# Kernel optimization log

Measured on AMD Instinct MI355X. Metric: run time of the kernel, lower is better.

Reference implementation:

```python
import jax, jax.numpy as jnp
import numpy as np

ATT = 512  # attention_size

def setup_inputs() -> dict:
    key = jax.random.key(0)
    k0, k1, k2, k3, k4 = jax.random.split(key, 5)
    B, Sq, Sk, Din, Dmem = 32, 1024, 1024, 512, 512
    inputs = jax.random.normal(k0, (B, Sq, Din), dtype=jnp.float32)
    memory = jax.random.normal(k1, (B, Sk, Dmem), dtype=jnp.float32)
    memory_mask = jax.random.randint(k2, (B, Sk), 0, 2).astype(jnp.int32)
    W_input = (jax.random.normal(k3, (Din, ATT), dtype=jnp.float32) * 0.02)
    W_memory = (jax.random.normal(k4, (Dmem, ATT), dtype=jnp.float32) * 0.02)
    return {"inputs": inputs, "memory": memory, "memory_mask": memory_mask,
            "W_input": W_input, "W_memory": W_memory}

def reference(inputs, memory, memory_mask, W_input, W_memory):
    # projections (bias=False) + ReLU; dropout=0 -> identity
    x = jax.nn.relu(jnp.einsum('bqd,da->bqa', inputs, W_input))   # [B,Sq,A]
    m = jax.nn.relu(jnp.einsum('bkd,da->bka', memory, W_memory))  # [B,Sk,A]
    scale = 1.0 / jnp.sqrt(jnp.asarray(ATT, dtype=inputs.dtype))
    logits = jnp.einsum('bqa,bka->bqk', x, m) * scale             # [B,Sq,Sk]
    mask = (memory_mask[:, None, :] != 0)                         # [B,1,Sk] broadcast over Sq
    logits = jnp.where(mask, logits, jnp.asarray(-1e30, dtype=logits.dtype))
    score = jax.nn.softmax(logits, axis=-1)
    context = jnp.einsum('bqk,bkd->bqd', score, memory)           # [B,Sq,Dmem]
    return jnp.concatenate([context, inputs], axis=-1)            # [B,Sq,Dmem+Din]
```

## Files before the change

### kernel.cpp

```cpp
#include <hip/hip_runtime.h>

typedef __bf16 bf16x8 __attribute__((ext_vector_type(8)));
typedef float f32x4 __attribute__((ext_vector_type(4)));

__device__ __forceinline__ unsigned short f2bf(float f) {
    union { float f; unsigned u; } v; v.f = f;
    unsigned r = v.u + 0x7FFFu + ((v.u >> 16) & 1u);
    return (unsigned short)(r >> 16);
}

__global__ __launch_bounds__(256) void prep_kernel(
    const float4* __restrict__ inputs4, uint2* __restrict__ InB16,
    float4* __restrict__ out4,
    const float* __restrict__ W0, const float* __restrict__ W1,
    unsigned short* __restrict__ D0, unsigned short* __restrict__ D1,
    const int* __restrict__ mask, int* __restrict__ kidx,
    int* __restrict__ cnt, int* __restrict__ padded,
    float4* __restrict__ rowsum4)
{
    __shared__ float tile[32][33];
    __shared__ int wsum[4];
    const int bid = blockIdx.x;
    const int t = threadIdx.x;

    if (bid < 16384) {
        const int i = bid * 256 + t;
        const int bq = i >> 7;
        const int d  = i & 127;
        float4 v = inputs4[i];
        out4[(size_t)bq * 256 + 128 + d] = v;
        union { unsigned short u[4]; uint2 p; } pk;
        pk.u[0] = f2bf(v.x); pk.u[1] = f2bf(v.y);
        pk.u[2] = f2bf(v.z); pk.u[3] = f2bf(v.w);
        InB16[i] = pk.p;
    } else if (bid < 16896) {
        const int tb = bid - 16384;
        const float* src = (tb >> 8) ? W1 : W0;
        unsigned short* dst = (tb >> 8) ? D1 : D0;
        const int rem = tb & 255;
        const int s0 = (rem & 15) * 32, d0 = (rem >> 4) * 32;
        const int tr = t >> 5, tc = t & 31;
#pragma unroll
        for (int i = 0; i < 4; i++)
            tile[tr + i * 8][tc] = src[(size_t)(s0 + tr + i * 8) * 512 + d0 + tc];
        __syncthreads();
#pragma unroll
        for (int i = 0; i < 4; i++)
            dst[(size_t)(d0 + tr + i * 8) * 512 + s0 + tc] = f2bf(tile[tc][tr + i * 8]);
    } else {
        const int b = bid - 16896;
        rowsum4[b * 256 + t] = float4{0.f, 0.f, 0.f, 0.f};
        const int* m = mask + b * 1024;
        int v[4]; int s = 0;
#pragma unroll
        for (int e = 0; e < 4; e++) { v[e] = (m[t * 4 + e] != 0) ? 1 : 0; s += v[e]; }
        const int lane = t & 63, wv = t >> 6;
        int x = s;
#pragma unroll
        for (int off = 1; off < 64; off <<= 1) {
            int y = __shfl_up(x, off, 64);
            if (lane >= off) x += y;
        }
        if (lane == 63) wsum[wv] = x;
        __syncthreads();
        int base = 0;
        for (int w = 0; w < wv; w++) base += wsum[w];
        int pos = base + x - s;
#pragma unroll
        for (int e = 0; e < 4; e++)
            if (v[e]) kidx[b * 1024 + pos++] = t * 4 + e;
        if (t == 255) {
            int total = base + x;
            cnt[b] = total;
            padded[b] = (total + 127) & ~127;
        }
    }
}

__global__ __launch_bounds__(256) void gather_mem_kernel(
    const float* __restrict__ memory, const int* __restrict__ kidx,
    const int* __restrict__ cnt, const int* __restrict__ padded,
    unsigned short* __restrict__ MemG, unsigned short* __restrict__ MemGT)
{
    const int b = blockIdx.z;
    const int j0 = blockIdx.x * 32, d0 = blockIdx.y * 32;
    if (j0 >= padded[b]) return;
    const int nb = cnt[b];
    __shared__ float tile[32][33];
    const float* src = memory + (size_t)b * 1024 * 512;
    const int t = threadIdx.x, tr = t >> 5, tc = t & 31;
#pragma unroll
    for (int i = 0; i < 4; i++) {
        int j = j0 + tr + i * 8;
        float v = 0.f;
        if (j < nb) v = src[(size_t)kidx[b * 1024 + j] * 512 + d0 + tc];
        tile[tr + i * 8][tc] = v;
        MemG[(size_t)b * 1024 * 512 + (size_t)j * 512 + d0 + tc] = f2bf(v);
    }
    __syncthreads();
#pragma unroll
    for (int i = 0; i < 4; i++) {
        int d = d0 + tr + i * 8;
        MemGT[(size_t)b * 512 * 1024 + (size_t)d * 1024 + j0 + tc] = f2bf(tile[tc][tr + i * 8]);
    }
}

template<int CMODE>
__device__ __forceinline__ void gemm_core(
    unsigned char* lds,
    const unsigned short* __restrict__ Ab, const unsigned short* __restrict__ Bb,
    void* __restrict__ Cb, float* __restrict__ rs, int nbv,
    int rowA, int rowB, int Kz, int lda, int ldb, int ldc, float scale)
{
    const int nt = Kz >> 6;

    const int t = threadIdx.x;
    const int w = t >> 6;
    const int lane = t & 63;
    const int wm = w >> 2;
    const int wn = w & 3;
    const int l15 = lane & 15;
    const int sx = (((lane >> 4) ^ ((l15 >> 1) & 3)) << 4);

    const int r0 = t >> 2;
    const int sl = (t & 3) ^ ((t >> 3) & 3);
    const unsigned short* aS0 = Ab + (size_t)(rowA + r0) * lda + sl * 8;
    const unsigned short* aS1 = aS0 + (size_t)128 * lda;
    const unsigned short* bS0 = Bb + (size_t)(rowB + r0) * ldb + sl * 8;
    const unsigned short* bS1 = bS0 + (size_t)128 * ldb;

    const int wofs = w * 1024;
    const int aRd = (wm * 128 + l15) * 64 + sx;
    const int bRd = 32768 + (wn * 64 + l15) * 64 + sx;

    f32x4 acc[8][4];
#pragma unroll
    for (int i = 0; i < 8; i++)
#pragma unroll
        for (int j = 0; j < 4; j++) acc[i][j] = f32x4{0.f, 0.f, 0.f, 0.f};

#define GLL(SRC, DOFS) __builtin_amdgcn_global_load_lds(                        \
        (const __attribute__((address_space(1))) void*)(SRC),                   \
        (__attribute__((address_space(3))) void*)&lds[DOFS], 16, 0, 0)
#define STAGEA(BUF, KH, KEL) do {                                               \
        GLL(aS0 + (KEL), (BUF) * 65536 + (KH) * 16384 + wofs);                  \
        GLL(aS1 + (KEL), (BUF) * 65536 + (KH) * 16384 + wofs + 8192); } while (0)
#define STAGEB(BUF, KH, KEL) do {                                               \
        GLL(bS0 + (KEL), (BUF) * 65536 + 32768 + (KH) * 16384 + wofs);          \
        GLL(bS1 + (KEL), (BUF) * 65536 + 32768 + (KH) * 16384 + wofs + 8192); } while (0)

    STAGEA(0, 0, 0); STAGEB(0, 0, 0); STAGEA(0, 1, 32); STAGEB(0, 1, 32);
    asm volatile("s_waitcnt vmcnt(4)" ::: "memory");
    __builtin_amdgcn_s_barrier();

    for (int tt = 0; tt < nt; ++tt) {
        const int cur = (tt & 1) * 65536;
        const int nxt = (tt & 1) ^ 1;
        const bool pf = (tt + 1) < nt;
        const int kn = (tt + 1) * 64;
        bf16x8 af[4], bf0[4], bf1[4];

#pragma unroll
        for (int i = 0; i < 4; i++) af[i]  = *(const bf16x8*)&lds[cur + aRd + i * 1024];
#pragma unroll
        for (int j = 0; j < 4; j++) bf0[j] = *(const bf16x8*)&lds[cur + bRd + j * 1024];
        if (pf) STAGEA(nxt, 0, kn);
        __builtin_amdgcn_s_barrier();
        asm volatile("s_waitcnt lgkmcnt(0)" ::: "memory");
        __builtin_amdgcn_sched_barrier(0);
        __builtin_amdgcn_s_setprio(1);
#pragma unroll
        for (int i = 0; i < 4; i++)
#pragma unroll
            for (int j = 0; j < 4; j++)
                acc[i][j] = __builtin_amdgcn_mfma_f32_16x16x32_bf16(af[i], bf0[j], acc[i][j], 0, 0, 0);
        __builtin_amdgcn_s_setprio(0);
        __builtin_amdgcn_s_barrier();

#pragma unroll
        for (int i = 0; i < 4; i++) af[i] = *(const bf16x8*)&lds[cur + aRd + (i + 4) * 1024];
        if (pf) STAGEB(nxt, 0, kn);
        __builtin_amdgcn_s_barrier();
        asm volatile("s_waitcnt lgkmcnt(0)" ::: "memory");
        __builtin_amdgcn_sched_barrier(0);
        __builtin_amdgcn_s_setprio(1);
#pragma unroll
        for (int i = 0; i < 4; i++)
#pragma unroll
            for (int j = 0; j < 4; j++)
                acc[i + 4][j] = __builtin_amdgcn_mfma_f32_16x16x32_bf16(af[i], bf0[j], acc[i + 4][j], 0, 0, 0);
        __builtin_amdgcn_s_setprio(0);
        if (pf) { asm volatile("s_waitcnt vmcnt(4)" ::: "memory"); }
        else    { asm volatile("s_waitcnt vmcnt(0)" ::: "memory"); }
        __builtin_amdgcn_s_barrier();

#pragma unroll
        for (int i = 0; i < 4; i++) af[i]  = *(const bf16x8*)&lds[cur + 16384 + aRd + i * 1024];
#pragma unroll
        for (int j = 0; j < 4; j++) bf1[j] = *(const bf16x8*)&lds[cur + 16384 + bRd + j * 1024];
        if (pf) STAGEA(nxt, 1, kn + 32);
        __builtin_amdgcn_s_barrier();
        asm volatile("s_waitcnt lgkmcnt(0)" ::: "memory");
        __builtin_amdgcn_sched_barrier(0);
        __builtin_amdgcn_s_setprio(1);
#pragma unroll
        for (int i = 0; i < 4; i++)
#pragma unroll
            for (int j = 0; j < 4; j++)
                acc[i][j] = __builtin_amdgcn_mfma_f32_16x16x32_bf16(af[i], bf1[j], acc[i][j], 0, 0, 0);
        __builtin_amdgcn_s_setprio(0);
        __builtin_amdgcn_s_barrier();

#pragma unroll
        for (int i = 0; i < 4; i++) af[i] = *(const bf16x8*)&lds[cur + 16384 + aRd + (i + 4) * 1024];
        if (pf) STAGEB(nxt, 1, kn + 32);
        __builtin_amdgcn_s_barrier();
        asm volatile("s_waitcnt lgkmcnt(0)" ::: "memory");
        __builtin_amdgcn_sched_barrier(0);
        __builtin_amdgcn_s_setprio(1);
#pragma unroll
        for (int i = 0; i < 4; i++)
#pragma unroll
            for (int j = 0; j < 4; j++)
                acc[i + 4][j] = __builtin_amdgcn_mfma_f32_16x16x32_bf16(af[i], bf1[j], acc[i + 4][j], 0, 0, 0);
        __builtin_amdgcn_s_setprio(0);
        if (pf) { asm volatile("s_waitcnt vmcnt(4)" ::: "memory"); }
        __builtin_amdgcn_s_barrier();
    }

#undef GLL
#undef STAGEA
#undef STAGEB

    const int orow = (lane >> 4) * 4;
    const int ocol = l15;

    if constexpr (CMODE == 0) {
        unsigned short* C = (unsigned short*)Cb;
#pragma unroll
        for (int mf = 0; mf < 8; mf++)
#pragma unroll
            for (int nf = 0; nf < 4; nf++) {
                const int col = rowB + wn * 64 + nf * 16 + ocol;
#pragma unroll
                for (int r = 0; r < 4; r++) {
                    const int rw = rowA + wm * 128 + mf * 16 + orow + r;
                    C[(size_t)rw * ldc + col] = f2bf(fmaxf(acc[mf][nf][r], 0.f));
                }
            }
    } else if constexpr (CMODE == 1) {
        unsigned short* C = (unsigned short*)Cb;
#pragma unroll
        for (int mf = 0; mf < 8; mf++) {
            float part[4] = {0.f, 0.f, 0.f, 0.f};
#pragma unroll
            for (int nf = 0; nf < 4; nf++) {
                const int col = rowB + wn * 64 + nf * 16 + ocol;
#pragma unroll
                for (int r = 0; r < 4; r++) {
                    float p = (col < nbv) ? __expf(acc[mf][nf][r] * scale) : 0.f;
                    part[r] += p;
                    const int rw = rowA + wm * 128 + mf * 16 + orow + r;
                    C[(size_t)rw * ldc + col] = f2bf(p);
                }
            }
#pragma unroll
            for (int r = 0; r < 4; r++) {
                float s = part[r];
                s += __shfl_xor(s, 1, 64);
                s += __shfl_xor(s, 2, 64);
                s += __shfl_xor(s, 4, 64);
                s += __shfl_xor(s, 8, 64);
                if (ocol == 0)
                    atomicAdd(&rs[rowA + wm * 128 + mf * 16 + orow + r], s);
            }
        }
    } else {
        float* C = (float*)Cb;
#pragma unroll
        for (int mf = 0; mf < 8; mf++) {
            float inv[4];
#pragma unroll
            for (int r = 0; r < 4; r++)
                inv[r] = 1.0f / rs[rowA + wm * 128 + mf * 16 + orow + r];
#pragma unroll
            for (int nf = 0; nf < 4; nf++) {
                const int col = rowB + wn * 64 + nf * 16 + ocol;
#pragma unroll
                for (int r = 0; r < 4; r++) {
                    const int rw = rowA + wm * 128 + mf * 16 + orow + r;
                    C[(size_t)rw * ldc + col] = acc[mf][nf][r] * inv[r];
                }
            }
        }
    }
}

__global__ __launch_bounds__(512, 2) void gemm_proj_kernel(
    const unsigned short* __restrict__ InB16, const unsigned short* __restrict__ WtIn,
    unsigned short* __restrict__ Xq,
    const unsigned short* __restrict__ MemG, const unsigned short* __restrict__ WtMem,
    unsigned short* __restrict__ Xm, const int* __restrict__ padded)
{
    __shared__ __align__(16) unsigned char lds[131072];
    const int y = blockIdx.y;
    const int rowB = blockIdx.x * 256;
    const unsigned short* A;
    const unsigned short* Bt;
    unsigned short* C;
    int rowA;
    if (y < 128) {
        A = InB16; Bt = WtIn; C = Xq; rowA = y * 256;
    } else {
        const int idx = y - 128;
        const int z = idx >> 2;
        rowA = (idx & 3) * 256;
        if (rowA >= padded[z]) return;
        A = MemG + (size_t)z * 524288;
        Bt = WtMem;
        C = Xm + (size_t)z * 524288;
    }
    gemm_core<0>(lds, A, Bt, (void*)C, nullptr, 0, rowA, rowB,
                 512, 512, 512, 512, 0.f);
}

__global__ __launch_bounds__(512, 2) void gemm_p_kernel(
    const unsigned short* __restrict__ Xq, const unsigned short* __restrict__ Xm,
    unsigned short* __restrict__ P, const int* __restrict__ cnt,
    const int* __restrict__ padded, float* __restrict__ rowsum, float scale)
{
    __shared__ __align__(16) unsigned char lds[131072];
    const int z = blockIdx.z;
    const int rowB = blockIdx.x * 256;
    if (rowB >= padded[z]) return;
    gemm_core<1>(lds, Xq + (size_t)z * 524288, Xm + (size_t)z * 524288,
                 (void*)(P + (size_t)z * 1048576), rowsum + (size_t)z * 1024, cnt[z],
                 blockIdx.y * 256, rowB, 512, 512, 512, 1024, scale);
}

__global__ __launch_bounds__(512, 2) void gemm_ctx_kernel(
    const unsigned short* __restrict__ P, const unsigned short* __restrict__ MemGT,
    float* __restrict__ out, const int* __restrict__ padded, float* __restrict__ rowsum)
{
    __shared__ __align__(16) unsigned char lds[131072];
    const int z = blockIdx.z;
    gemm_core<2>(lds, P + (size_t)z * 1048576, MemGT + (size_t)z * 524288,
                 (void*)(out + (size_t)z * 1048576), rowsum + (size_t)z * 1024, 0,
                 blockIdx.y * 256, blockIdx.x * 256, padded[z],
                 1024, 1024, 1024, 1.f);
}

extern "C" void kernel_launch(void* const* d_in, const int* in_sizes, int n_in,
                              void* d_out, int out_size, void* d_ws, size_t ws_size,
                              hipStream_t stream)
{
    const float* inputs = (const float*)d_in[0];
    const float* memory = (const float*)d_in[1];
    const int*   mmask  = (const int*)d_in[2];
    const float* W_in   = (const float*)d_in[3];
    const float* W_mem  = (const float*)d_in[4];
    float* out = (float*)d_out;

    char* ws = (char*)d_ws;
    const unsigned long long MB = 1048576ull;
    unsigned short* Wt_in  = (unsigned short*)(ws);
    unsigned short* Wt_mem = (unsigned short*)(ws + 524288);
    unsigned short* InB16  = (unsigned short*)(ws + 1 * MB);
    unsigned short* MemG   = (unsigned short*)(ws + 33 * MB);
    unsigned short* P      = (unsigned short*)(ws + 1 * MB);
    unsigned short* MemGT  = (unsigned short*)(ws + 65 * MB);
    unsigned short* Xq     = (unsigned short*)(ws + 97 * MB);
    unsigned short* Xm     = (unsigned short*)(ws + 129 * MB);
    float*          rowsum = (float*)(ws + 161 * MB);
    int*            kidx   = (int*)(ws + 161 * MB + 131072);
    int*            cntp   = (int*)(ws + 161 * MB + 262144);
    int*            padp   = (int*)(ws + 161 * MB + 262144 + 128);

    const float scale = 0.04419417382415922f;

    prep_kernel<<<16928, 256, 0, stream>>>(
        (const float4*)inputs, (uint2*)InB16, (float4*)out,
        W_in, W_mem, Wt_in, Wt_mem,
        mmask, kidx, cntp, padp, (float4*)rowsum);

    gather_mem_kernel<<<dim3(32, 16, 32), 256, 0, stream>>>(
        memory, kidx, cntp, padp, MemG, MemGT);

    gemm_proj_kernel<<<dim3(2, 256, 1), 512, 0, stream>>>(
        InB16, Wt_in, Xq, MemG, Wt_mem, Xm, padp);

    gemm_p_kernel<<<dim3(4, 4, 32), 512, 0, stream>>>(
        Xq, Xm, P, cntp, padp, rowsum, scale);

    gemm_ctx_kernel<<<dim3(2, 4, 32), 512, 0, stream>>>(
        P, MemGT, out, padp, rowsum);
}
```

Baseline: 398.6 us.

## Fuse mask compaction and memory gather into prep kernel; XCD-aware block remapping

```diff
diff --git a/kernel.cpp b/kernel.cpp
--- a/kernel.cpp
+++ b/kernel.cpp
@@ -14,17 +14,107 @@
     float4* __restrict__ out4,
     const float* __restrict__ W0, const float* __restrict__ W1,
     unsigned short* __restrict__ D0, unsigned short* __restrict__ D1,
-    const int* __restrict__ mask, int* __restrict__ kidx,
+    const int* __restrict__ mask,
     int* __restrict__ cnt, int* __restrict__ padded,
-    float4* __restrict__ rowsum4)
+    float4* __restrict__ rowsum4,
+    const float* __restrict__ memory,
+    unsigned short* __restrict__ MemG, unsigned short* __restrict__ MemGT)
 {
     __shared__ float tile[32][33];
     __shared__ int wsum[4];
+    __shared__ int kidx32[32];
     const int bid = blockIdx.x;
     const int t = threadIdx.x;
 
-    if (bid < 16384) {
-        const int i = bid * 256 + t;
+    if (bid < 1024) {
+        const int b = bid >> 5;
+        const int jt = bid & 31;
+        const int* m = mask + b * 1024;
+        int v[4]; int s = 0;
+#pragma unroll
+        for (int e = 0; e < 4; e++) { v[e] = (m[t * 4 + e] != 0) ? 1 : 0; s += v[e]; }
+        const int lane = t & 63, wv = t >> 6;
+        int x = s;
+#pragma unroll
+        for (int off = 1; off < 64; off <<= 1) {
+            int y = __shfl_up(x, off, 64);
+            if (lane >= off) x += y;
+        }
+        if (lane == 63) wsum[wv] = x;
+        __syncthreads();
+        int base = 0;
+        for (int w = 0; w < wv; w++) base += wsum[w];
+        const int nb = wsum[0] + wsum[1] + wsum[2] + wsum[3];
+        const int pb = (nb + 127) & ~127;
+        const int j0 = jt * 32;
+        if (j0 >= pb) return;
+        int pos = base + x - s;
+#pragma unroll
+        for (int e = 0; e < 4; e++)
+            if (v[e]) {
+                int p = pos++;
+                if (p >= j0 && p < j0 + 32) kidx32[p - j0] = t * 4 + e;
+            }
+        __syncthreads();
+
+        const float* src = memory + (size_t)b * 1024 * 512;
+        const int tr = t >> 5, tc = t & 31;
+        for (int d0 = 0; d0 < 512; d0 += 32) {
+#pragma unroll
+            for (int i = 0; i < 4; i++) {
+                const int jj = tr + i * 8;
+                const int j = j0 + jj;
+                float vv = 0.f;
+                if (j < nb) vv = src[(size_t)kidx32[jj] * 512 + d0 + tc];
+                tile[jj][tc] = vv;
+                MemG[(size_t)b * 1024 * 512 + (size_t)j * 512 + d0 + tc] = f2bf(vv);
+            }
+            __syncthreads();
+#pragma unroll
+            for (int i = 0; i < 4; i++) {
+                const int d = d0 + tr + i * 8;
+                MemGT[(size_t)b * 512 * 1024 + (size_t)d * 1024 + j0 + tc] =
+                    f2bf(tile[tc][tr + i * 8]);
+            }
+            __syncthreads();
+        }
+    } else if (bid < 1056) {
+        const int b = bid - 1024;
+        rowsum4[b * 256 + t] = float4{0.f, 0.f, 0.f, 0.f};
+        const int* m = mask + b * 1024;
+        int s = 0;
+#pragma unroll
+        for (int e = 0; e < 4; e++) s += (m[t * 4 + e] != 0) ? 1 : 0;
+        const int lane = t & 63, wv = t >> 6;
+        int x = s;
+#pragma unroll
+        for (int off = 1; off < 64; off <<= 1) {
+            int y = __shfl_up(x, off, 64);
+            if (lane >= off) x += y;
+        }
+        if (lane == 63) wsum[wv] = x;
+        __syncthreads();
+        if (t == 255) {
+            int total = wsum[0] + wsum[1] + wsum[2] + wsum[3];
+            cnt[b] = total;
+            padded[b] = (total + 127) & ~127;
+        }
+    } else if (bid < 1568) {
+        const int tb = bid - 1056;
+        const float* src = (tb >> 8) ? W1 : W0;
+        unsigned short* dst = (tb >> 8) ? D1 : D0;
+        const int rem = tb & 255;
+        const int s0 = (rem & 15) * 32, d0 = (rem >> 4) * 32;
+        const int tr = t >> 5, tc = t & 31;
+#pragma unroll
+        for (int i = 0; i < 4; i++)
+            tile[tr + i * 8][tc] = src[(size_t)(s0 + tr + i * 8) * 512 + d0 + tc];
+        __syncthreads();
+#pragma unroll
+        for (int i = 0; i < 4; i++)
+            dst[(size_t)(d0 + tr + i * 8) * 512 + s0 + tc] = f2bf(tile[tc][tr + i * 8]);
+    } else {
+        const int i = (bid - 1568) * 256 + t;
         const int bq = i >> 7;
         const int d  = i & 127;
         float4 v = inputs4[i];
@@ -33,75 +123,6 @@
         pk.u[0] = f2bf(v.x); pk.u[1] = f2bf(v.y);
         pk.u[2] = f2bf(v.z); pk.u[3] = f2bf(v.w);
         InB16[i] = pk.p;
-    } else if (bid < 16896) {
-        const int tb = bid - 16384;
-        const float* src = (tb >> 8) ? W1 : W0;
-        unsigned short* dst = (tb >> 8) ? D1 : D0;
-        const int rem = tb & 255;
-        const int s0 = (rem & 15) * 32, d0 = (rem >> 4) * 32;
-        const int tr = t >> 5, tc = t & 31;
-#pragma unroll
-        for (int i = 0; i < 4; i++)
-            tile[tr + i * 8][tc] = src[(size_t)(s0 + tr + i * 8) * 512 + d0 + tc];
-        __syncthreads();
-#pragma unroll
-        for (int i = 0; i < 4; i++)
-            dst[(size_t)(d0 + tr + i * 8) * 512 + s0 + tc] = f2bf(tile[tc][tr + i * 8]);
-    } else {
-        const int b = bid - 16896;
-        rowsum4[b * 256 + t] = float4{0.f, 0.f, 0.f, 0.f};
-        const int* m = mask + b * 1024;
-        int v[4]; int s = 0;
-#pragma unroll
-        for (int e = 0; e < 4; e++) { v[e] = (m[t * 4 + e] != 0) ? 1 : 0; s += v[e]; }
-        const int lane = t & 63, wv = t >> 6;
-        int x = s;
-#pragma unroll
-        for (int off = 1; off < 64; off <<= 1) {
-            int y = __shfl_up(x, off, 64);
-            if (lane >= off) x += y;
-        }
-        if (lane == 63) wsum[wv] = x;
-        __syncthreads();
-        int base = 0;
-        for (int w = 0; w < wv; w++) base += wsum[w];
-        int pos = base + x - s;
-#pragma unroll
-        for (int e = 0; e < 4; e++)
-            if (v[e]) kidx[b * 1024 + pos++] = t * 4 + e;
-        if (t == 255) {
-            int total = base + x;
-            cnt[b] = total;
-            padded[b] = (total + 127) & ~127;
-        }
-    }
-}
-
-__global__ __launch_bounds__(256) void gather_mem_kernel(
-    const float* __restrict__ memory, const int* __restrict__ kidx,
-    const int* __restrict__ cnt, const int* __restrict__ padded,
-    unsigned short* __restrict__ MemG, unsigned short* __restrict__ MemGT)
-{
-    const int b = blockIdx.z;
-    const int j0 = blockIdx.x * 32, d0 = blockIdx.y * 32;
-    if (j0 >= padded[b]) return;
-    const int nb = cnt[b];
-    __shared__ float tile[32][33];
-    const float* src = memory + (size_t)b * 1024 * 512;
-    const int t = threadIdx.x, tr = t >> 5, tc = t & 31;
-#pragma unroll
-    for (int i = 0; i < 4; i++) {
-        int j = j0 + tr + i * 8;
-        float v = 0.f;
-        if (j < nb) v = src[(size_t)kidx[b * 1024 + j] * 512 + d0 + tc];
-        tile[tr + i * 8][tc] = v;
-        MemG[(size_t)b * 1024 * 512 + (size_t)j * 512 + d0 + tc] = f2bf(v);
-    }
-    __syncthreads();
-#pragma unroll
-    for (int i = 0; i < 4; i++) {
-        int d = d0 + tr + i * 8;
-        MemGT[(size_t)b * 512 * 1024 + (size_t)d * 1024 + j0 + tc] = f2bf(tile[tc][tr + i * 8]);
     }
 }
 
@@ -303,8 +324,11 @@
     unsigned short* __restrict__ Xm, const int* __restrict__ padded)
 {
     __shared__ __align__(16) unsigned char lds[131072];
-    const int y = blockIdx.y;
-    const int rowB = blockIdx.x * 256;
+    const int id = blockIdx.x;
+    const int xcd = id & 7, slot = id >> 3;
+    const int y = xcd + 8 * (slot >> 1);
+    const int x = slot & 1;
+    const int rowB = x * 256;
     const unsigned short* A;
     const unsigned short* Bt;
     unsigned short* C;
@@ -330,12 +354,16 @@
     const int* __restrict__ padded, float* __restrict__ rowsum, float scale)
 {
     __shared__ __align__(16) unsigned char lds[131072];
-    const int z = blockIdx.z;
-    const int rowB = blockIdx.x * 256;
+    const int id = blockIdx.x;
+    const int xcd = id & 7, slot = id >> 3;
+    const int z = xcd + 8 * (slot >> 4);
+    const int r = slot & 15;
+    const int x = r & 3, y = r >> 2;
+    const int rowB = x * 256;
     if (rowB >= padded[z]) return;
     gemm_core<1>(lds, Xq + (size_t)z * 524288, Xm + (size_t)z * 524288,
                  (void*)(P + (size_t)z * 1048576), rowsum + (size_t)z * 1024, cnt[z],
-                 blockIdx.y * 256, rowB, 512, 512, 512, 1024, scale);
+                 y * 256, rowB, 512, 512, 512, 1024, scale);
 }
 
 __global__ __launch_bounds__(512, 2) void gemm_ctx_kernel(
@@ -343,10 +371,14 @@
     float* __restrict__ out, const int* __restrict__ padded, float* __restrict__ rowsum)
 {
     __shared__ __align__(16) unsigned char lds[131072];
-    const int z = blockIdx.z;
+    const int id = blockIdx.x;
+    const int xcd = id & 7, slot = id >> 3;
+    const int z = xcd + 8 * (slot >> 3);
+    const int r = slot & 7;
+    const int x = r & 1, y = r >> 1;
     gemm_core<2>(lds, P + (size_t)z * 1048576, MemGT + (size_t)z * 524288,
                  (void*)(out + (size_t)z * 1048576), rowsum + (size_t)z * 1024, 0,
-                 blockIdx.y * 256, blockIdx.x * 256, padded[z],
+                 y * 256, x * 256, padded[z],
                  1024, 1024, 1024, 1.f);
 }
 
@@ -372,26 +404,23 @@
     unsigned short* Xq     = (unsigned short*)(ws + 97 * MB);
     unsigned short* Xm     = (unsigned short*)(ws + 129 * MB);
     float*          rowsum = (float*)(ws + 161 * MB);
-    int*            kidx   = (int*)(ws + 161 * MB + 131072);
     int*            cntp   = (int*)(ws + 161 * MB + 262144);
     int*            padp   = (int*)(ws + 161 * MB + 262144 + 128);
 
     const float scale = 0.04419417382415922f;
 
-    prep_kernel<<<16928, 256, 0, stream>>>(
+    prep_kernel<<<17952, 256, 0, stream>>>(
         (const float4*)inputs, (uint2*)InB16, (float4*)out,
         W_in, W_mem, Wt_in, Wt_mem,
-        mmask, kidx, cntp, padp, (float4*)rowsum);
-
-    gather_mem_kernel<<<dim3(32, 16, 32), 256, 0, stream>>>(
-        memory, kidx, cntp, padp, MemG, MemGT);
-
-    gemm_proj_kernel<<<dim3(2, 256, 1), 512, 0, stream>>>(
+        mmask, cntp, padp, (float4*)rowsum,
+        memory, MemG, MemGT);
+
+    gemm_proj_kernel<<<512, 512, 0, stream>>>(
         InB16, Wt_in, Xq, MemG, Wt_mem, Xm, padp);
 
-    gemm_p_kernel<<<dim3(4, 4, 32), 512, 0, stream>>>(
+    gemm_p_kernel<<<512, 512, 0, stream>>>(
         Xq, Xm, P, cntp, padp, rowsum, scale);
 
-    gemm_ctx_kernel<<<dim3(2, 4, 32), 512, 0, stream>>>(
+    gemm_ctx_kernel<<<256, 512, 0, stream>>>(
         P, MemGT, out, padp, rowsum);
 }
```

Result: faster. 376.5 us (-5.5%).
